# Performance work log

Measured on AMD Instinct MI355X. Metric: run time of the kernel, lower is better.

The kernel has to match this reference:

```python
import jax, jax.numpy as jnp
import numpy as np


def _conv(x, w, b, pad):
    y = jax.lax.conv_general_dilated(x, w, (1, 1), [(pad, pad), (pad, pad)],
                                     dimension_numbers=('NCHW', 'OIHW', 'NCHW'))
    return y + b[None, :, None, None]


def _group_norm(x, gamma, beta, groups=4, eps=1e-5):
    B, C, H, W = x.shape
    xg = x.reshape(B, groups, C // groups, H, W)
    mu = xg.mean(axis=(2, 3, 4), keepdims=True)
    var = ((xg - mu) ** 2).mean(axis=(2, 3, 4), keepdims=True)
    xn = ((xg - mu) * jax.lax.rsqrt(var + eps)).reshape(B, C, H, W)
    return xn * gamma[None, :, None, None] + beta[None, :, None, None]


def _deform_conv2d(x, offsets, weight, bias, pad=1):
    # torchvision-style deform_conv2d, stride=1, dilation=1, 1 offset group.
    # x: [B,C,H,W]; offsets: [B,2*9,H,W] interleaved (dy,dx) per 3x3 tap (row-major).
    B, C, H, W = x.shape
    K = 9
    off = offsets.reshape(B, K, 2, H, W)
    ki = jnp.arange(3)
    gi = jnp.repeat(ki, 3).astype(x.dtype)  # kernel row index per tap
    gj = jnp.tile(ki, 3).astype(x.dtype)    # kernel col index per tap
    # sampling position: p = p_out + (k - pad) + offset
    py = off[:, :, 0] + jnp.arange(H, dtype=x.dtype)[None, None, :, None] + (gi - pad)[None, :, None, None]
    px = off[:, :, 1] + jnp.arange(W, dtype=x.dtype)[None, None, None, :] + (gj - pad)[None, :, None, None]
    y0 = jnp.floor(py)
    x0 = jnp.floor(px)
    wy1 = py - y0  # [B,K,H,W]
    wx1 = px - x0
    xf = x.reshape(B, C, H * W)

    def gather(yi, xi):
        valid = (yi >= 0) & (yi < H) & (xi >= 0) & (xi < W)
        yc = jnp.clip(yi, 0, H - 1).astype(jnp.int32)
        xc = jnp.clip(xi, 0, W - 1).astype(jnp.int32)
        idx = (yc * W + xc).reshape(B, 1, K * H * W)
        v = jnp.take_along_axis(xf, idx, axis=2).reshape(B, C, K, H, W)
        return v * valid.astype(x.dtype)[:, None]  # zero-pad outside

    sampled = (gather(y0, x0) * ((1 - wy1) * (1 - wx1))[:, None]
               + gather(y0, x0 + 1) * ((1 - wy1) * wx1)[:, None]
               + gather(y0 + 1, x0) * (wy1 * (1 - wx1))[:, None]
               + gather(y0 + 1, x0 + 1) * (wy1 * wx1)[:, None])  # [B,C,K,H,W]
    out = jnp.einsum('bckhw,ock->bohw', sampled, weight.reshape(weight.shape[0], C, K))
    return out + bias[None, :, None, None]


def setup_inputs() -> dict:
    key = jax.random.key(0)
    ks = jax.random.split(key, 8)
    B, C, H, W = 8, 256, 128, 128
    mid = max(C // 4, 32)  # 64
    f32 = jnp.float32
    return {
        "features": jax.random.normal(ks[0], (B, C, H, W), f32),
        "wind_uv": jax.random.normal(ks[1], (B, 2, H, W), f32),
        "compress_w": jax.random.normal(ks[2], (mid, C, 1, 1), f32) * 0.05,
        "compress_b": jnp.zeros((mid,), f32),
        "off1_w": jax.random.normal(ks[3], (32, 2, 3, 3), f32) * 0.1,
        "off1_b": jnp.zeros((32,), f32),
        "off2_w": jax.random.normal(ks[4], (18, 32, 3, 3), f32) * 0.05,
        "off2_b": jnp.zeros((18,), f32),
        "deform_w": jax.random.normal(ks[5], (mid, mid, 3, 3), f32) * 0.02,
        "deform_b": jnp.zeros((mid,), f32),
        "expand_w": jax.random.normal(ks[6], (C, mid, 1, 1), f32) * 0.05,
        "expand_b": jnp.zeros((C,), f32),
        "gn_gamma": jnp.ones((C,), f32),
        "gn_beta": jnp.zeros((C,), f32),
    }


def reference(features, wind_uv, compress_w, compress_b, off1_w, off1_b,
              off2_w, off2_b, deform_w, deform_b, expand_w, expand_b,
              gn_gamma, gn_beta):
    x = _conv(features, compress_w, compress_b, 0)
    h = jax.nn.gelu(_conv(wind_uv, off1_w, off1_b, 1), approximate=False)
    offsets = _conv(h, off2_w, off2_b, 1)
    x = _deform_conv2d(x, offsets, deform_w, deform_b, pad=1)
    x = _conv(x, expand_w, expand_b, 0)
    return features + jax.nn.gelu(_group_norm(x, gn_gamma, gn_beta), approximate=False)
```

## Files before the change

kernel.cpp:

```cpp
#include <hip/hip_runtime.h>
#include <math.h>


#define BB 8
#define CC 256
#define HW 16384
#define MID 64

typedef __attribute__((ext_vector_type(8))) short bf16x8;
typedef __attribute__((ext_vector_type(4))) float f32x4;

__device__ __forceinline__ float gelu_f(float v){
  return 0.5f*v*(1.0f + erff(v*0.7071067811865476f));
}
__device__ __forceinline__ unsigned f2bf(float f){
  union { float f; unsigned u; } v; v.f = f;
  unsigned u = v.u;
  u += 0x7fff + ((u >> 16) & 1);
  return (u >> 16);
}
__device__ __forceinline__ float bf2f(unsigned u){
  union { unsigned u; float f; } v; v.u = u; return v.f;
}

__global__ void k_prep(const float* __restrict__ dw, const float* __restrict__ cw,
                       const float* __restrict__ ew, ushort* __restrict__ bt,
                       ushort* __restrict__ cwb, ushort* __restrict__ ewb){
  int i = blockIdx.x*256 + threadIdx.x;
  if (i < 36864){
    int k = i >> 12, r = i & 4095;
    int o = r >> 6, c = r & 63;
    bt[i] = (ushort)f2bf(dw[(o*64+c)*9 + k]);
  }
  int j = i - 36864;
  if (j >= 0 && j < 16384) cwb[j] = (ushort)f2bf(cw[j]);
  int l = i - 53248;
  if (l >= 0 && l < 16384) ewb[l] = (ushort)f2bf(ew[l]);
}

__global__ __launch_bounds__(256) void k_compress(const float* __restrict__ feat,
    const ushort* __restrict__ cwb, const float* __restrict__ cb, float* __restrict__ xo){
  __shared__ ushort A[128*64];
  int t = threadIdx.x;
  int b = blockIdx.y, p0 = blockIdx.x*128;
  int lane = t & 63, w = t >> 6, ln = lane & 15, qd = lane >> 4;
  int n = (w<<4) + ln;
  int cg = t >> 4, pxg = t & 15;
  f32x4 acc[8];
  #pragma unroll
  for (int pt=0;pt<8;pt++) acc[pt] = (f32x4){0.f,0.f,0.f,0.f};
  for (int kt=0;kt<4;kt++){
    const float* fb = feat + ((size_t)(b*CC + kt*64 + cg*4))*HW + p0 + pxg*8;
    float v[4][8];
    #pragma unroll
    for (int i=0;i<4;i++){
      *(float4*)&v[i][0] = *(const float4*)(fb + (size_t)i*HW);
      *(float4*)&v[i][4] = *(const float4*)(fb + (size_t)i*HW + 4);
    }
    __syncthreads();
    #pragma unroll
    for (int j=0;j<8;j++){
      int px = pxg*8 + j;
      unsigned lo = f2bf(v[0][j]) | (f2bf(v[1][j])<<16);
      unsigned hi = f2bf(v[2][j]) | (f2bf(v[3][j])<<16);
      int chunk = (cg>>1) ^ (px&7);
      *(uint2*)((char*)A + px*128 + chunk*16 + (cg&1)*8) = make_uint2(lo,hi);
    }
    __syncthreads();
    const ushort* wb = cwb + (size_t)n*256 + kt*64 + (qd<<3);
    bf16x8 b0 = *(const bf16x8*)wb;
    bf16x8 b1 = *(const bf16x8*)(wb + 32);
    #pragma unroll
    for (int pt=0;pt<8;pt++){
      int m = (pt<<4) + ln;
      int ch0 = qd ^ (m&7), ch1 = (4+qd) ^ (m&7);
      bf16x8 a0 = *(bf16x8*)(A + (m<<6) + (ch0<<3));
      acc[pt] = __builtin_amdgcn_mfma_f32_16x16x32_bf16(a0, b0, acc[pt], 0,0,0);
      bf16x8 a1 = *(bf16x8*)(A + (m<<6) + (ch1<<3));
      acc[pt] = __builtin_amdgcn_mfma_f32_16x16x32_bf16(a1, b1, acc[pt], 0,0,0);
    }
  }
  float bias = cb[n];
  float* xp = xo + ((size_t)(b*HW + p0))*64 + n;
  #pragma unroll
  for (int pt=0;pt<8;pt++){
    #pragma unroll
    for (int rg=0;rg<4;rg++){
      int px = (pt<<4) + (qd<<2) + rg;
      xp[(size_t)px*64] = acc[pt][rg] + bias;
    }
  }
}

__global__ __launch_bounds__(256) void k_off1(const float* __restrict__ wind,
    const float* __restrict__ w1, const float* __restrict__ b1, float* __restrict__ ho){
  __shared__ float wl[576];
  int t=threadIdx.x;
  for (int i=t;i<576;i+=256) wl[i]=w1[i];
  __syncthreads();
  int b=blockIdx.y; int p=blockIdx.x*256+t;
  int y=p>>7, x=p&127;
  float tap[18];
  #pragma unroll
  for (int c=0;c<2;c++){
    #pragma unroll
    for (int ki=0;ki<3;ki++){
      #pragma unroll
      for (int kj=0;kj<3;kj++){
        int yy=y+ki-1, xx=x+kj-1;
        float v=0.f;
        if ((unsigned)yy<128u && (unsigned)xx<128u)
          v = wind[((size_t)b*2+c)*HW + (yy<<7)+xx];
        tap[c*9+ki*3+kj]=v;
      }
    }
  }
  float outv[32];
  #pragma unroll
  for (int o=0;o<32;o++){
    float a=b1[o];
    #pragma unroll
    for (int i=0;i<18;i++) a += tap[i]*wl[o*18+i];
    outv[o]=gelu_f(a);
  }
  float* hp = ho + ((size_t)(b*HW+p))*32;
  #pragma unroll
  for (int o=0;o<32;o+=4) *(float4*)(hp+o)=make_float4(outv[o],outv[o+1],outv[o+2],outv[o+3]);
}

__global__ __launch_bounds__(256) void k_off2(const float* __restrict__ h,
    const float* __restrict__ w2, const float* __restrict__ b2, float* __restrict__ oo){
  __shared__ float wl[9*18*32];
  int t=threadIdx.x;
  for (int i=t;i<5184;i+=256){
    int k=i/576; int r=i-k*576; int o=r>>5; int c=r&31;
    wl[i] = w2[(o*32+c)*9+k];
  }
  __syncthreads();
  int b=blockIdx.y; int p=blockIdx.x*256+t;
  int y=p>>7, x=p&127;
  float acc[18];
  #pragma unroll
  for (int o=0;o<18;o++) acc[o]=b2[o];
  for (int ki=0;ki<3;ki++){
    for (int kj=0;kj<3;kj++){
      int k = ki*3+kj;
      int yy=y+ki-1, xx=x+kj-1;
      float4 hv[8];
      if ((unsigned)yy<128u && (unsigned)xx<128u){
        const float* hp = h + ((size_t)(b*HW) + (yy<<7)+xx)*32;
        #pragma unroll
        for (int q=0;q<8;q++) hv[q]=*(const float4*)(hp+q*4);
      } else {
        #pragma unroll
        for (int q=0;q<8;q++) hv[q]=make_float4(0.f,0.f,0.f,0.f);
      }
      const float* wk = &wl[k*576];
      #pragma unroll
      for (int o=0;o<18;o++){
        float a=acc[o];
        #pragma unroll
        for (int q=0;q<8;q++){
          float4 w4 = *(const float4*)(wk + o*32 + q*4);
          a += hv[q].x*w4.x + hv[q].y*w4.y + hv[q].z*w4.z + hv[q].w*w4.w;
        }
        acc[o]=a;
      }
    }
  }
  float* op = oo + ((size_t)(b*HW+p))*18;
  #pragma unroll
  for (int o=0;o<18;o+=2) *(float2*)(op+o)=make_float2(acc[o],acc[o+1]);
}

__global__ __launch_bounds__(256) void k_deform(
    const float* __restrict__ x, const float* __restrict__ off,
    const ushort* __restrict__ bt, const float* __restrict__ db,
    ushort* __restrict__ yo, float* __restrict__ partY2,
    float* __restrict__ partYb){
  __shared__ ushort A[128*64];
  __shared__ float offs[128*18];
  int t = threadIdx.x;
  int blk = blockIdx.x;
  int b = blk & 7, r = blk >> 3;
  int p0 = r*128;
  const float* offg = off + ((size_t)(b*HW + p0))*18;
  for (int i=t;i<576;i+=256)
    *(float4*)(offs + i*4) = *(const float4*)(offg + i*4);
  __syncthreads();
  int lane = t & 63, w = t >> 6, ln = lane & 15, qd = lane >> 4;
  int n = (w<<4) + ln;
  const float* xb = x + (size_t)b*HW*64;
  f32x4 acc[8];
  #pragma unroll
  for (int pt=0;pt<8;pt++) acc[pt] = (f32x4){0.f,0.f,0.f,0.f};

  for (int k=0;k<9;k++){
    int ki = k/3, kj = k - ki*3;
    const ushort* btk = bt + (size_t)(((k<<6) + n)<<6) + (qd<<3);
    bf16x8 bf0 = *(const bf16x8*)btk;
    bf16x8 bf1 = *(const bf16x8*)(btk + 32);
    __syncthreads();
    #pragma unroll
    for (int pp=0;pp<8;pp++){
      int p = (w<<5) + (pp<<2) + qd;
      float2 dd = *(const float2*)(offs + p*18 + 2*k);
      float py  = dd.x + (float)(r + ki - 1);
      float pxs = dd.y + (float)(p + kj - 1);
      float y0f = floorf(py), x0f = floorf(pxs);
      float fy = py - y0f, fx = pxs - x0f;
      int y0 = (int)y0f, x0 = (int)x0f;
      float w00=(1.f-fy)*(1.f-fx), w01=(1.f-fy)*fx, w10=fy*(1.f-fx), w11=fy*fx;
      bool v0=((unsigned)y0<128u), v1=((unsigned)(y0+1)<128u);
      bool u0=((unsigned)x0<128u), u1=((unsigned)(x0+1)<128u);
      w00 = (v0&&u0)? w00 : 0.f;  w01 = (v0&&u1)? w01 : 0.f;
      w10 = (v1&&u0)? w10 : 0.f;  w11 = (v1&&u1)? w11 : 0.f;
      int y0c = min(max(y0,0),127), y1c = min(max(y0+1,0),127);
      int x0c = min(max(x0,0),127), x1c = min(max(x0+1,0),127);
      int cofs = (ln<<2);
      const float4* r00 = (const float4*)(xb + (size_t)y0c*8192 + x0c*64 + cofs);
      const float4* r01 = (const float4*)(xb + (size_t)y0c*8192 + x1c*64 + cofs);
      const float4* r10 = (const float4*)(xb + (size_t)y1c*8192 + x0c*64 + cofs);
      const float4* r11 = (const float4*)(xb + (size_t)y1c*8192 + x1c*64 + cofs);
      float4 a00=*r00, a01=*r01, a10=*r10, a11=*r11;
      float4 s;
      s.x = a00.x*w00 + a01.x*w01 + a10.x*w10 + a11.x*w11;
      s.y = a00.y*w00 + a01.y*w01 + a10.y*w10 + a11.y*w11;
      s.z = a00.z*w00 + a01.z*w01 + a10.z*w10 + a11.z*w11;
      s.w = a00.w*w00 + a01.w*w01 + a10.w*w10 + a11.w*w11;
      unsigned lo = f2bf(s.x) | (f2bf(s.y)<<16);
      unsigned hi = f2bf(s.z) | (f2bf(s.w)<<16);
      int chunk = (ln>>1) ^ (p&7);
      *(uint2*)((char*)A + p*128 + chunk*16 + (ln&1)*8) = make_uint2(lo,hi);
    }
    __syncthreads();
    #pragma unroll
    for (int pt=0;pt<8;pt++){
      int m = (pt<<4) + ln;
      int ch0 = qd ^ (m&7), ch1 = (4+qd) ^ (m&7);
      bf16x8 a0 = *(bf16x8*)(A + (m<<6) + (ch0<<3));
      acc[pt] = __builtin_amdgcn_mfma_f32_16x16x32_bf16(a0, bf0, acc[pt], 0,0,0);
      bf16x8 a1 = *(bf16x8*)(A + (m<<6) + (ch1<<3));
      acc[pt] = __builtin_amdgcn_mfma_f32_16x16x32_bf16(a1, bf1, acc[pt], 0,0,0);
    }
  }
  __syncthreads();
  float bias = db[n];
  float ysum = 0.f;
  #pragma unroll
  for (int pt=0;pt<8;pt++){
    #pragma unroll
    for (int rg=0;rg<4;rg++){
      int px = (pt<<4) + (qd<<2) + rg;
      float yv = acc[pt][rg] + bias;
      A[(px<<6) + n] = (ushort)f2bf(yv);
      ysum += yv;
    }
  }
  ysum += __shfl_xor(ysum, 16, 64);
  ysum += __shfl_xor(ysum, 32, 64);
  __syncthreads();
  uint4* yq = (uint4*)(yo + ((size_t)(b*HW + p0))*64);
  const uint4* As = (const uint4*)A;
  #pragma unroll
  for (int q=0;q<4;q++) yq[t + q*256] = As[t + q*256];
  if (qd == 0) partYb[((size_t)(b*128+r))*64 + n] = ysum;
  int ib = t & 15, jb = t >> 4;
  float sacc[4][4];
  #pragma unroll
  for (int a=0;a<4;a++)
    #pragma unroll
    for (int c=0;c<4;c++) sacc[a][c]=0.f;
  for (int p=0;p<128;p++){
    uint2 ui = *(const uint2*)(A + (p<<6) + (ib<<2));
    uint2 uj = *(const uint2*)(A + (p<<6) + (jb<<2));
    float fi[4] = { bf2f(ui.x<<16), bf2f(ui.x&0xffff0000u),
                    bf2f(ui.y<<16), bf2f(ui.y&0xffff0000u) };
    float fj[4] = { bf2f(uj.x<<16), bf2f(uj.x&0xffff0000u),
                    bf2f(uj.y<<16), bf2f(uj.y&0xffff0000u) };
    #pragma unroll
    for (int a=0;a<4;a++)
      #pragma unroll
      for (int c=0;c<4;c++) sacc[a][c] += fi[a]*fj[c];
  }
  float* pb = partY2 + ((size_t)(b*128+r))*4096;
  #pragma unroll
  for (int a=0;a<4;a++)
    *(float4*)(pb + (ib*4+a)*64 + jb*4) =
        make_float4(sacc[a][0],sacc[a][1],sacc[a][2],sacc[a][3]);
}

__global__ __launch_bounds__(256) void k_reduce(const float* __restrict__ partY2,
    const float* __restrict__ partYb, float* __restrict__ YQ,
    float* __restrict__ ybar){
  int t=threadIdx.x; int b=blockIdx.y;
  if (blockIdx.x < 16){
    int eq = blockIdx.x >> 2, rq = blockIdx.x & 3;
    int e = (eq*256 + t)*4;
    const float* p = partY2 + ((size_t)(b*128 + rq*32))*4096 + e;
    float4 s=make_float4(0.f,0.f,0.f,0.f);
    for (int r=0;r<32;r++){
      float4 v=*(const float4*)(p+(size_t)r*4096);
      s.x+=v.x; s.y+=v.y; s.z+=v.z; s.w+=v.w;
    }
    *(float4*)(YQ + (((size_t)(b*4 + rq))<<12) + e)=s;
  } else if (t < 16){
    int e = t*4;
    const float* p = partYb + (size_t)b*8192 + e;
    float4 s=make_float4(0.f,0.f,0.f,0.f);
    for (int r=0;r<128;r++){
      float4 v=*(const float4*)(p+r*64);
      s.x+=v.x; s.y+=v.y; s.z+=v.z; s.w+=v.w;
    }
    *(float4*)(ybar+(b<<6)+e)=s;
  }
}

__global__ __launch_bounds__(256) void k_gn(const float* __restrict__ YQ,
    const float* __restrict__ ybar, const float* __restrict__ ew,
    const float* __restrict__ eb, float* __restrict__ stats){
  __shared__ float wsm[64*65];
  __shared__ float red[512];
  int t=threadIdx.x;
  int bg=blockIdx.x, b=bg>>2, g=bg&3;
  for (int i=t;i<4096;i+=256){
    int c=i>>6, m=i&63;
    wsm[c*65+m] = ew[(((size_t)g<<6)+c)*64 + m];
  }
  __syncthreads();
  int c = t&63, qm = t>>6;
  const float* wv = &wsm[c*65];
  const float* Y2b = YQ + ((size_t)(b*4)<<12);
  const float* yb = ybar + (b<<6);
  float q=0.f, sbp=0.f;
  for (int m=qm*16; m<qm*16+16; m++){
    const float* row = Y2b + (m<<6);
    float ym=0.f;
    for (int nn=0;nn<64;nn+=4){
      float4 a0=*(const float4*)(row+nn);
      float4 a1=*(const float4*)(row+4096+nn);
      float4 a2=*(const float4*)(row+8192+nn);
      float4 a3=*(const float4*)(row+12288+nn);
      float sx=a0.x+a1.x+a2.x+a3.x;
      float sy=a0.y+a1.y+a2.y+a3.y;
      float sz=a0.z+a1.z+a2.z+a3.z;
      float sw=a0.w+a1.w+a2.w+a3.w;
      ym += sx*wv[nn] + sy*wv[nn+1] + sz*wv[nn+2] + sw*wv[nn+3];
    }
    q += ym*wv[m];
    sbp += wv[m]*yb[m];
  }
  float bias = eb[(g<<6)+c];
  float pz  = sbp + (qm==0 ? 16384.f*bias : 0.f);
  float pz2 = q + 2.f*bias*sbp + (qm==0 ? 16384.f*bias*bias : 0.f);
  red[t]=pz; red[256+t]=pz2;
  __syncthreads();
  for (int s=128;s>0;s>>=1){
    if (t<s){ red[t]+=red[t+s]; red[256+t]+=red[256+t+s]; }
    __syncthreads();
  }
  if (t==0){
    const float N=64.f*16384.f;
    float mu = red[0]/N;
    float var = red[256]/N - mu*mu;
    stats[bg*2]=mu; stats[bg*2+1]=rsqrtf(var+1e-5f);
  }
}

__global__ __launch_bounds__(256) void k_final(const ushort* __restrict__ y,
    const ushort* __restrict__ ewb, const float* __restrict__ eb,
    const float* __restrict__ stats, const float* __restrict__ gamma,
    const float* __restrict__ beta, const float* __restrict__ feat,
    float* __restrict__ out){
  __shared__ ushort A[64*64];
  int t = threadIdx.x;
  int b = blockIdx.y, p0 = blockIdx.x*64;
  int lane = t & 63, w = t >> 6, ln = lane & 15, qd = lane >> 4;
  {
    int px = t>>2, ch0 = (t&3)*16;
    const uint4* yp = (const uint4*)(y + ((size_t)(b*HW + p0 + px))*64 + ch0);
    uint4 v0 = yp[0], v1 = yp[1];
    int c16 = ch0 >> 3;
    char* Ab = (char*)A + px*128;
    *(uint4*)(Ab + ((c16  )^(px&7))*16) = v0;
    *(uint4*)(Ab + ((c16+1)^(px&7))*16) = v1;
  }
  __syncthreads();
  float mu = stats[((b<<2)+w)*2], rstd = stats[((b<<2)+w)*2+1];
  const float* fb = feat + (size_t)b*CC*HW + p0;
  float* ob = out + (size_t)b*CC*HW + p0;
  f32x4 fpre[4];
  {
    const float* frow = fb + (size_t)((w<<6) + ln)*HW;
    #pragma unroll
    for (int pt=0;pt<4;pt++)
      fpre[pt] = *(const f32x4*)(frow + (pt<<4) + (qd<<2));
  }
  #pragma unroll
  for (int nt=0;nt<4;nt++){
    int nch = (w<<6) + (nt<<4) + ln;
    const ushort* wb = ewb + (size_t)nch*64 + (qd<<3);
    bf16x8 b0 = *(const bf16x8*)wb;
    bf16x8 b1 = *(const bf16x8*)(wb + 32);
    f32x4 acc[4];
    #pragma unroll
    for (int pt=0;pt<4;pt++) acc[pt] = (f32x4){0.f,0.f,0.f,0.f};
    #pragma unroll
    for (int pt=0;pt<4;pt++){
      int m = (pt<<4) + ln;
      int ch0 = qd ^ (m&7), ch1 = (4+qd) ^ (m&7);
      bf16x8 a0 = *(bf16x8*)(A + (m<<6) + (ch0<<3));
      acc[pt] = __builtin_amdgcn_mfma_f32_16x16x32_bf16(a0, b0, acc[pt], 0,0,0);
      bf16x8 a1 = *(bf16x8*)(A + (m<<6) + (ch1<<3));
      acc[pt] = __builtin_amdgcn_mfma_f32_16x16x32_bf16(a1, b1, acc[pt], 0,0,0);
    }
    f32x4 fcur[4];
    #pragma unroll
    for (int pt=0;pt<4;pt++) fcur[pt] = fpre[pt];
    if (nt < 3){
      const float* frow = fb + (size_t)(nch + 16)*HW;
      #pragma unroll
      for (int pt=0;pt<4;pt++)
        fpre[pt] = *(const f32x4*)(frow + (pt<<4) + (qd<<2));
    }
    float bias = eb[nch];
    float ga = gamma[nch], be = beta[nch];
    float gr = rstd*ga;
    float ofs = (bias - mu)*gr + be;
    float* orow = ob + (size_t)nch*HW;
    #pragma unroll
    for (int pt=0;pt<4;pt++){
      int px = (pt<<4) + (qd<<2);
      f32x4 f = fcur[pt];
      f32x4 o;
      o[0] = f[0] + gelu_f(acc[pt][0]*gr + ofs);
      o[1] = f[1] + gelu_f(acc[pt][1]*gr + ofs);
      o[2] = f[2] + gelu_f(acc[pt][2]*gr + ofs);
      o[3] = f[3] + gelu_f(acc[pt][3]*gr + ofs);
      __builtin_nontemporal_store(o, (f32x4*)(orow + px));
    }
  }
}

extern "C" void kernel_launch(void* const* d_in, const int* in_sizes, int n_in,
                              void* d_out, int out_size, void* d_ws, size_t ws_size,
                              hipStream_t stream){
  const float* feat = (const float*)d_in[0];
  const float* wind = (const float*)d_in[1];
  const float* cw   = (const float*)d_in[2];
  const float* cb   = (const float*)d_in[3];
  const float* w1   = (const float*)d_in[4];
  const float* b1   = (const float*)d_in[5];
  const float* w2   = (const float*)d_in[6];
  const float* b2   = (const float*)d_in[7];
  const float* dw   = (const float*)d_in[8];
  const float* db   = (const float*)d_in[9];
  const float* ew   = (const float*)d_in[10];
  const float* ebias= (const float*)d_in[11];
  const float* gg   = (const float*)d_in[12];
  const float* gb   = (const float*)d_in[13];
  float* ws = (float*)d_ws;
  float* x_nhwc   = ws;
  ushort* y_bf16  = (ushort*)(ws + 8388608);
  float* h_nhwc   = ws + 16777216;
  float* off_nhwc = ws + 20971520;
  ushort* bt      = (ushort*)(ws + 23330816);
  ushort* cwb     = (ushort*)(ws + 23349248);
  ushort* ewb     = (ushort*)(ws + 23357440);
  float* ybar     = ws + 23398400;
  float* stats    = ws + 23398912;
  float* partY2   = h_nhwc;
  float* partYb   = off_nhwc;
  float* YQ       = off_nhwc + 131072;
  k_prep<<<272,256,0,stream>>>(dw, cw, ew, bt, cwb, ewb);
  k_compress<<<dim3(128,8),256,0,stream>>>(feat, cwb, cb, x_nhwc);
  k_off1<<<dim3(64,8),256,0,stream>>>(wind, w1, b1, h_nhwc);
  k_off2<<<dim3(64,8),256,0,stream>>>(h_nhwc, w2, b2, off_nhwc);
  k_deform<<<1024,256,0,stream>>>(x_nhwc, off_nhwc, bt, db, y_bf16, partY2, partYb);
  k_reduce<<<dim3(17,8),256,0,stream>>>(partY2, partYb, YQ, ybar);
  k_gn<<<32,256,0,stream>>>(YQ, ybar, ew, ebias, stats);
  k_final<<<dim3(256,8),256,0,stream>>>(y_bf16, ewb, ebias, stats, gg, gb, feat, (float*)d_out);
}
```

Before: 488.1 us.

## Have each wave own its pixel rows in deform MFMA to drop block barriers

Before, each wave computed all 128 pixels for its own 16 output channels, which needed two block-wide barriers per tap. Now each wave computes its own 32 pixel rows across all 64 channels, so it only reads the A tile rows it wrote itself. That removes the per-tap __syncthreads and lets waves overlap gather work with MFMA work. In exchange, each wave loads four times the B-fragment data from global memory per tap, and the per-channel sums are now reduced across waves through shared memory. The partYb and YQ buffers are moved to a separate workspace region, likely so they no longer alias offsets that other blocks are still reading.

```diff
diff --git a/kernel.cpp b/kernel.cpp
--- a/kernel.cpp
+++ b/kernel.cpp
@@ -189,21 +189,19 @@
     *(float4*)(offs + i*4) = *(const float4*)(offg + i*4);
   __syncthreads();
   int lane = t & 63, w = t >> 6, ln = lane & 15, qd = lane >> 4;
-  int n = (w<<4) + ln;
+  int wpx0 = w << 5;
   const float* xb = x + (size_t)b*HW*64;
-  f32x4 acc[8];
-  #pragma unroll
-  for (int pt=0;pt<8;pt++) acc[pt] = (f32x4){0.f,0.f,0.f,0.f};
+  f32x4 acc[2][4];
+  #pragma unroll
+  for (int i=0;i<2;i++)
+    #pragma unroll
+    for (int j=0;j<4;j++) acc[i][j] = (f32x4){0.f,0.f,0.f,0.f};
 
   for (int k=0;k<9;k++){
     int ki = k/3, kj = k - ki*3;
-    const ushort* btk = bt + (size_t)(((k<<6) + n)<<6) + (qd<<3);
-    bf16x8 bf0 = *(const bf16x8*)btk;
-    bf16x8 bf1 = *(const bf16x8*)(btk + 32);
-    __syncthreads();
     #pragma unroll
     for (int pp=0;pp<8;pp++){
-      int p = (w<<5) + (pp<<2) + qd;
+      int p = wpx0 + (pp<<2) + qd;
       float2 dd = *(const float2*)(offs + p*18 + 2*k);
       float py  = dd.x + (float)(r + ki - 1);
       float pxs = dd.y + (float)(p + kj - 1);
@@ -233,38 +231,57 @@
       int chunk = (ln>>1) ^ (p&7);
       *(uint2*)((char*)A + p*128 + chunk*16 + (ln&1)*8) = make_uint2(lo,hi);
     }
-    __syncthreads();
-    #pragma unroll
-    for (int pt=0;pt<8;pt++){
-      int m = (pt<<4) + ln;
-      int ch0 = qd ^ (m&7), ch1 = (4+qd) ^ (m&7);
-      bf16x8 a0 = *(bf16x8*)(A + (m<<6) + (ch0<<3));
-      acc[pt] = __builtin_amdgcn_mfma_f32_16x16x32_bf16(a0, bf0, acc[pt], 0,0,0);
-      bf16x8 a1 = *(bf16x8*)(A + (m<<6) + (ch1<<3));
-      acc[pt] = __builtin_amdgcn_mfma_f32_16x16x32_bf16(a1, bf1, acc[pt], 0,0,0);
-    }
-  }
-  __syncthreads();
-  float bias = db[n];
-  float ysum = 0.f;
-  #pragma unroll
-  for (int pt=0;pt<8;pt++){
+    #pragma unroll
+    for (int nt=0;nt<4;nt++){
+      int n = (nt<<4) + ln;
+      const ushort* btk = bt + (size_t)(((k<<6) + n)<<6) + (qd<<3);
+      bf16x8 bf0 = *(const bf16x8*)btk;
+      bf16x8 bf1 = *(const bf16x8*)(btk + 32);
+      #pragma unroll
+      for (int pxt=0;pxt<2;pxt++){
+        int m = wpx0 + (pxt<<4) + ln;
+        int ch0 = qd ^ (m&7), ch1 = (4+qd) ^ (m&7);
+        bf16x8 a0 = *(bf16x8*)(A + (m<<6) + (ch0<<3));
+        acc[pxt][nt] = __builtin_amdgcn_mfma_f32_16x16x32_bf16(a0, bf0, acc[pxt][nt], 0,0,0);
+        bf16x8 a1 = *(bf16x8*)(A + (m<<6) + (ch1<<3));
+        acc[pxt][nt] = __builtin_amdgcn_mfma_f32_16x16x32_bf16(a1, bf1, acc[pxt][nt], 0,0,0);
+      }
+    }
+  }
+  float bias[4], ysum[4];
+  #pragma unroll
+  for (int nt=0;nt<4;nt++){ bias[nt] = db[(nt<<4)+ln]; ysum[nt]=0.f; }
+  #pragma unroll
+  for (int pxt=0;pxt<2;pxt++){
     #pragma unroll
     for (int rg=0;rg<4;rg++){
-      int px = (pt<<4) + (qd<<2) + rg;
-      float yv = acc[pt][rg] + bias;
-      A[(px<<6) + n] = (ushort)f2bf(yv);
-      ysum += yv;
-    }
-  }
-  ysum += __shfl_xor(ysum, 16, 64);
-  ysum += __shfl_xor(ysum, 32, 64);
+      int px = wpx0 + (pxt<<4) + (qd<<2) + rg;
+      #pragma unroll
+      for (int nt=0;nt<4;nt++){
+        float yv = acc[pxt][nt][rg] + bias[nt];
+        A[(px<<6) + (nt<<4) + ln] = (ushort)f2bf(yv);
+        ysum[nt] += yv;
+      }
+    }
+  }
+  #pragma unroll
+  for (int nt=0;nt<4;nt++){
+    ysum[nt] += __shfl_xor(ysum[nt], 16, 64);
+    ysum[nt] += __shfl_xor(ysum[nt], 32, 64);
+  }
+  __syncthreads();
+  if (qd == 0){
+    #pragma unroll
+    for (int nt=0;nt<4;nt++) offs[(w<<6) + (nt<<4) + ln] = ysum[nt];
+  }
   __syncthreads();
   uint4* yq = (uint4*)(yo + ((size_t)(b*HW + p0))*64);
   const uint4* As = (const uint4*)A;
   #pragma unroll
   for (int q=0;q<4;q++) yq[t + q*256] = As[t + q*256];
-  if (qd == 0) partYb[((size_t)(b*128+r))*64 + n] = ysum;
+  if (t < 64)
+    partYb[((size_t)(b*128+r))*64 + t] =
+        offs[t] + offs[64+t] + offs[128+t] + offs[192+t];
   int ib = t & 15, jb = t >> 4;
   float sacc[4][4];
   #pragma unroll
@@ -462,6 +479,8 @@
   float* ws = (float*)d_ws;
   float* x_nhwc   = ws;
   ushort* y_bf16  = (ushort*)(ws + 8388608);
+  float* partYb   = ws + 12582912;
+  float* YQ       = ws + 12648448;
   float* h_nhwc   = ws + 16777216;
   float* off_nhwc = ws + 20971520;
   ushort* bt      = (ushort*)(ws + 23330816);
@@ -470,8 +489,6 @@
   float* ybar     = ws + 23398400;
   float* stats    = ws + 23398912;
   float* partY2   = h_nhwc;
-  float* partYb   = off_nhwc;
-  float* YQ       = off_nhwc + 131072;
   k_prep<<<272,256,0,stream>>>(dw, cw, ew, bt, cwb, ewb);
   k_compress<<<dim3(128,8),256,0,stream>>>(feat, cwb, cb, x_nhwc);
   k_off1<<<dim3(64,8),256,0,stream>>>(wind, w1, b1, h_nhwc);
```

Measured after the change: 541.4 us. +10.9%, slower.
